# Kernel tuning notes

Measured on AMD Instinct MI355X. Metric: run time of the kernel, lower is better.

Reference implementation:

```python
import jax, jax.numpy as jnp
from jax import lax
import numpy as np

B, IN, HID, OUT, E = 32768, 512, 1024, 2, 64
N_MEM, N_ITER = 100, 10


def setup_inputs() -> dict:
    key = jax.random.key(0)
    ks = jax.random.split(key, 10)
    x = jax.random.normal(ks[0], (B, IN), dtype=jnp.float32)
    # encoder params (Linear stored as [in, out] for x @ W + b)
    e_w1 = jax.random.normal(ks[1], (IN, HID), dtype=jnp.float32) * 0.02
    e_b1 = jnp.zeros((HID,), dtype=jnp.float32)
    e_w2 = jax.random.normal(ks[2], (HID, E), dtype=jnp.float32) * 0.02
    e_b2 = jnp.zeros((E,), dtype=jnp.float32)
    # Hopfield weights: sum of outer products of N_MEM bipolar memories, zero diag, /N_MEM
    mems = jnp.where(jax.random.bernoulli(ks[3], 0.5, (N_MEM, E)), 1.0, -1.0)
    hop_w = (mems.T @ mems) / N_MEM
    hop_w = hop_w * (1.0 - jnp.eye(E, dtype=jnp.float32))
    # Q-network params
    n_w1 = jax.random.normal(ks[4], (IN + E, HID), dtype=jnp.float32) * 0.02
    n_b1 = jnp.zeros((HID,), dtype=jnp.float32)
    n_w2 = jax.random.normal(ks[5], (HID, HID), dtype=jnp.float32) * 0.02
    n_b2 = jnp.zeros((HID,), dtype=jnp.float32)
    n_w3 = jax.random.normal(ks[6], (HID, OUT), dtype=jnp.float32) * 0.02
    n_b3 = jnp.zeros((OUT,), dtype=jnp.float32)
    return {"x": x, "e_w1": e_w1, "e_b1": e_b1, "e_w2": e_w2, "e_b2": e_b2,
            "hop_w": hop_w, "n_w1": n_w1, "n_b1": n_b1, "n_w2": n_w2,
            "n_b2": n_b2, "n_w3": n_w3, "n_b3": n_b3}


def _retrieve(probe, hop_w):
    # Asynchronous Hopfield retrieval, batched over B.
    # probe: [B, E]; state in {+1,-1}
    state = jnp.where(probe > 0, 1.0, -1.0)
    idxs = jnp.arange(E)

    def unit_step(state, xs):
        i, w_row = xs  # w_row: [E]
        act = state @ w_row  # [B]
        state = state.at[:, i].set(jnp.where(act > 0, 1.0, -1.0))
        return state, None

    def iter_body(state, _):
        state, _ = lax.scan(unit_step, state, (idxs, hop_w))
        return state, None

    state, _ = lax.scan(iter_body, state, None, length=N_ITER)
    return jnp.where(state > 0, 1.0, 0.0)


def reference(x, e_w1, e_b1, e_w2, e_b2, hop_w, n_w1, n_b1, n_w2, n_b2, n_w3, n_b3):
    encoded = jax.nn.relu(x @ e_w1 + e_b1) @ e_w2 + e_b2  # [B, E]
    retrieved = lax.stop_gradient(_retrieve(encoded, hop_w))  # detached in original
    combined = jnp.concatenate([x, retrieved], axis=1)  # [B, IN+E]
    h = jax.nn.relu(combined @ n_w1 + n_b1)
    h = jax.nn.relu(h @ n_w2 + n_b2)
    return h @ n_w3 + n_b3  # [B, OUT]
```

## Files before the change

kernel.cpp:

```cpp
#include <hip/hip_runtime.h>
#include <hip/hip_bf16.h>
#include <stdint.h>
#include <math.h>

typedef __attribute__((ext_vector_type(4))) float f32x4;
typedef __attribute__((ext_vector_type(8))) __bf16 bf16x8;
typedef __attribute__((ext_vector_type(8))) uint16_t u16x8;
typedef __attribute__((ext_vector_type(4))) uint32_t u32x4;

__device__ __forceinline__ uint16_t f2bf(float f) {
  union { float f; uint32_t u; } v; v.f = f;
  uint32_t r = v.u + 0x7FFFu + ((v.u >> 16) & 1u);
  return (uint16_t)(r >> 16);
}
__device__ __forceinline__ float bf2f(uint16_t b) {
  union { uint32_t u; float f; } v; v.u = ((uint32_t)b) << 16;
  return v.f;
}

__global__ __launch_bounds__(256) void k_conv_x(const float* __restrict__ x,
                                                uint16_t* __restrict__ comb) {
  int i = blockIdx.x * 256 + threadIdx.x;
  int base = i * 8;
  int row = base >> 9;
  int col = base & 511;
  const float* src = x + base;
  f32x4 a = *(const f32x4*)src;
  f32x4 b = *(const f32x4*)(src + 4);
  u16x8 o;
  o[0] = f2bf(a[0]); o[1] = f2bf(a[1]); o[2] = f2bf(a[2]); o[3] = f2bf(a[3]);
  o[4] = f2bf(b[0]); o[5] = f2bf(b[1]); o[6] = f2bf(b[2]); o[7] = f2bf(b[3]);
  *(u16x8*)(comb + (size_t)row * 576 + col) = o;
}

__global__ __launch_bounds__(256) void k_convT(const float* __restrict__ W,
                                               uint16_t* __restrict__ WT,
                                               int K, int N) {
  int i = blockIdx.x * 256 + threadIdx.x;
  if (i < K * N) {
    int k = i / N, n = i % N;
    WT[n * K + k] = f2bf(W[i]);
  }
}

__global__ __launch_bounds__(256) void k_conv(const float* __restrict__ W,
                                              uint16_t* __restrict__ O, int n) {
  int i = blockIdx.x * 256 + threadIdx.x;
  if (i < n) O[i] = f2bf(W[i]);
}

template <int K, bool RELU>
__global__ __launch_bounds__(256)
void k_enc(const float* __restrict__ A, const float* __restrict__ W,
           const float* __restrict__ bias, float* __restrict__ C, int N) {
  __shared__ __align__(16) float xs[64][136];
  __shared__ __align__(16) float ws[64][68];
  const int t = threadIdx.x;
  const int m0 = blockIdx.y * 128, n0 = blockIdx.x * 64;
  const int mg = t >> 4, ng = t & 15;

  float res[8][4], acc[8][4];
#pragma unroll
  for (int i = 0; i < 8; ++i)
#pragma unroll
    for (int j = 0; j < 4; ++j) { res[i][j] = 0.f; acc[i][j] = 0.f; }

  const int xr = t >> 1, xk = (t & 1) * 32;
  const int wrr = t >> 2, wj = (t & 3) * 16;

  for (int c = 0; c < K / 64; ++c) {
    const int k0 = c * 64;
    if (k0 > 0 && (k0 % 384) == 0) {
#pragma unroll
      for (int i = 0; i < 8; ++i)
#pragma unroll
        for (int j = 0; j < 4; ++j) { res[i][j] += acc[i][j]; acc[i][j] = 0.f; }
    }
    __syncthreads();
#pragma unroll
    for (int u = 0; u < 8; ++u) {
      f32x4 v = *(const f32x4*)(A + (size_t)(m0 + xr) * K + k0 + xk + u * 4);
      xs[xk + u * 4 + 0][xr] = v[0];
      xs[xk + u * 4 + 1][xr] = v[1];
      xs[xk + u * 4 + 2][xr] = v[2];
      xs[xk + u * 4 + 3][xr] = v[3];
    }
#pragma unroll
    for (int u = 0; u < 4; ++u)
      *(f32x4*)&ws[wrr][wj + u * 4] =
          *(const f32x4*)(W + (size_t)(k0 + wrr) * N + n0 + wj + u * 4);
    __syncthreads();
#pragma unroll
    for (int k = 0; k < 64; ++k) {
      f32x4 x0 = *(const f32x4*)&xs[k][mg * 8];
      f32x4 x1 = *(const f32x4*)&xs[k][mg * 8 + 4];
      f32x4 wv = *(const f32x4*)&ws[k][ng * 4];
#pragma unroll
      for (int j = 0; j < 4; ++j) {
        acc[0][j] = fmaf(x0[0], wv[j], acc[0][j]);
        acc[1][j] = fmaf(x0[1], wv[j], acc[1][j]);
        acc[2][j] = fmaf(x0[2], wv[j], acc[2][j]);
        acc[3][j] = fmaf(x0[3], wv[j], acc[3][j]);
        acc[4][j] = fmaf(x1[0], wv[j], acc[4][j]);
        acc[5][j] = fmaf(x1[1], wv[j], acc[5][j]);
        acc[6][j] = fmaf(x1[2], wv[j], acc[6][j]);
        acc[7][j] = fmaf(x1[3], wv[j], acc[7][j]);
      }
    }
  }
#pragma unroll
  for (int i = 0; i < 8; ++i)
#pragma unroll
    for (int j = 0; j < 4; ++j) res[i][j] += acc[i][j];

#pragma unroll
  for (int i = 0; i < 8; ++i) {
    f32x4 o;
#pragma unroll
    for (int j = 0; j < 4; ++j) {
      float v = res[i][j] + bias[n0 + ng * 4 + j];
      if (RELU) v = fmaxf(v, 0.f);
      o[j] = v;
    }
    *(f32x4*)(C + (size_t)(m0 + mg * 8 + i) * N + n0 + ng * 4) = o;
  }
}

#define KNIFE_TAU 1e-6f

__device__ __forceinline__ void retrieve8(float (&s)[8],
                                          const float (*w)[64], int l) {
  for (int it = 0; it < 10; ++it) {
    bool changed = false;
#pragma unroll
    for (int i = 0; i < 64; ++i) {
      float r = 0.f;
#pragma unroll
      for (int c = 0; c < 8; ++c)
        r = fmaf(s[c], w[i][8 * c + l], r);
      r += __shfl_xor(r, 1);
      r += __shfl_xor(r, 2);
      r += __shfl_xor(r, 4);
      float ns = r > 0.f ? 1.f : -1.f;
      bool own = ((i & 7) == l);
      float cur = s[i >> 3];
      float nv = own ? ns : cur;
      changed |= (nv != cur);
      s[i >> 3] = nv;
    }
    if (!__any(changed)) break;
  }
}

__device__ __forceinline__ uint64_t gather_mask(const float (&s)[8], int g) {
  uint64_t m = 0;
#pragma unroll
  for (int c = 0; c < 8; ++c) {
    unsigned long long b = __ballot(s[c] > 0.f);
    m |= (uint64_t)((b >> (g * 8)) & 0xFFull) << (8 * c);
  }
  return m;
}

__global__ __launch_bounds__(256) void k_hopfield(const float* __restrict__ enc,
                                                  const float* __restrict__ hw,
                                                  uint16_t* __restrict__ comb) {
  __shared__ __align__(16) float w[64][64];
  const int t = threadIdx.x;
#pragma unroll
  for (int i = 0; i < 4; ++i)
    ((f32x4*)&w[0][0])[t * 4 + i] = ((const f32x4*)hw)[t * 4 + i];
  __syncthreads();

  const int lane = t & 63, wv = t >> 6;
  const int g = lane >> 3, l = lane & 7;
  const int sid = (blockIdx.x * 4 + wv) * 8 + g;
  const float* er = enc + (size_t)sid * 64;

  uint32_t imask = 0;
  int kc = -1;
  bool kpos = false;
#pragma unroll
  for (int c = 0; c < 8; ++c) {
    float v = er[8 * c + l];
    if (v > 0.f) imask |= (1u << c);
    if (kc < 0 && fabsf(v) < KNIFE_TAU) { kc = c; kpos = v > 0.f; }
  }
  unsigned long long kb = __ballot(kc >= 0);
  uint32_t gbits = (uint32_t)((kb >> (g * 8)) & 0xFFull);
  bool hasknife = gbits != 0;
  int klane = g * 8 + (__ffs(gbits) - 1);
  bool is_kl = hasknife && (lane == klane);
  uint32_t kbit = (kc >= 0) ? (1u << (kc & 7)) : 0u;

  uint32_t ma_bits = is_kl ? (imask | kbit) : imask;
  float sA[8];
#pragma unroll
  for (int c = 0; c < 8; ++c) sA[c] = ((ma_bits >> c) & 1u) ? 1.f : -1.f;
  retrieve8(sA, w, l);
  uint64_t mA = gather_mask(sA, g);
  uint64_t m = mA;

  if (__any(hasknife)) {
    if (hasknife) {
      uint32_t mb_bits = is_kl ? (imask & ~kbit) : imask;
      float sB[8];
#pragma unroll
      for (int c = 0; c < 8; ++c) sB[c] = ((mb_bits >> c) & 1u) ? 1.f : -1.f;
      retrieve8(sB, w, l);
      uint64_t mB = gather_mask(sB, g);
      if (mA != mB) {
        int kp = __shfl(kpos ? 1 : 0, klane);
        m = kp ? mA : mB;
      }
    }
  }

  uint32_t byte = (uint32_t)((m >> (8 * l)) & 0xFFull);
  u32x4 o;
#pragma unroll
  for (int p = 0; p < 4; ++p) {
    uint32_t lo = ((byte >> (2 * p)) & 1u) ? 0x3F80u : 0u;
    uint32_t hi = ((byte >> (2 * p + 1)) & 1u) ? 0x3F800000u : 0u;
    o[p] = lo | hi;
  }
  *(u32x4*)(comb + (size_t)sid * 576 + 512 + l * 8) = o;
}

__global__ __launch_bounds__(256)
void k_gemm_bf16(const uint16_t* __restrict__ A, const uint16_t* __restrict__ BT,
                 const float* __restrict__ bias, uint16_t* __restrict__ C,
                 int M, int N, int K, int relu) {
  constexpr int BM = 128, BN = 128, BK = 32;
  __shared__ __align__(16) uint16_t As[BM][BK];
  __shared__ __align__(16) uint16_t Bs[BN][BK];
  const int t = threadIdx.x;
  const int lane = t & 63, wid = t >> 6;
  const int wr = wid >> 1, wc = wid & 1;
  const int bm = blockIdx.y * BM, bn = blockIdx.x * BN;

  f32x4 acc[4][4] = {};

  const int s_row = t >> 1, s_kh = (t & 1) * 16;
  const uint16_t* Ag = A + (size_t)(bm + s_row) * K + s_kh;
  const uint16_t* Bg = BT + (size_t)(bn + s_row) * K + s_kh;
  const int l15 = lane & 15, kb = (lane >> 4) * 8;

  for (int kt = 0; kt < K / BK; ++kt) {
    __syncthreads();
    u16x8 av0 = *(const u16x8*)(Ag + kt * BK);
    u16x8 av1 = *(const u16x8*)(Ag + kt * BK + 8);
    u16x8 bv0 = *(const u16x8*)(Bg + kt * BK);
    u16x8 bv1 = *(const u16x8*)(Bg + kt * BK + 8);
    *(u16x8*)&As[s_row][s_kh] = av0;
    *(u16x8*)&As[s_row][s_kh + 8] = av1;
    *(u16x8*)&Bs[s_row][s_kh] = bv0;
    *(u16x8*)&Bs[s_row][s_kh + 8] = bv1;
    __syncthreads();
    bf16x8 af[4], bf[4];
#pragma unroll
    for (int m = 0; m < 4; ++m)
      af[m] = *(const bf16x8*)&As[wr * 64 + m * 16 + l15][kb];
#pragma unroll
    for (int n = 0; n < 4; ++n)
      bf[n] = *(const bf16x8*)&Bs[wc * 64 + n * 16 + l15][kb];
#pragma unroll
    for (int m = 0; m < 4; ++m)
#pragma unroll
      for (int n = 0; n < 4; ++n)
        acc[m][n] = __builtin_amdgcn_mfma_f32_16x16x32_bf16(af[m], bf[n],
                                                            acc[m][n], 0, 0, 0);
  }
#pragma unroll
  for (int m = 0; m < 4; ++m) {
    int row = bm + wr * 64 + m * 16 + (lane >> 4) * 4;
#pragma unroll
    for (int n = 0; n < 4; ++n) {
      int col = bn + wc * 64 + n * 16 + l15;
      float bsv = bias[col];
#pragma unroll
      for (int r = 0; r < 4; ++r) {
        float v = acc[m][n][r] + bsv;
        if (relu) v = fmaxf(v, 0.f);
        C[(size_t)(row + r) * N + col] = f2bf(v);
      }
    }
  }
}

__global__ __launch_bounds__(256) void k_n3(const uint16_t* __restrict__ h2,
                                            const uint16_t* __restrict__ w3,
                                            const float* __restrict__ b3,
                                            float* __restrict__ out, int M) {
  const int lane = threadIdx.x & 63;
  const int wglob = (blockIdx.x * 256 + threadIdx.x) >> 6;
  const int nw = (gridDim.x * 256) >> 6;
  u16x8 wa = *(const u16x8*)(w3 + lane * 16);
  u16x8 wb = *(const u16x8*)(w3 + lane * 16 + 8);
  u16x8 wc = *(const u16x8*)(w3 + 1024 + lane * 16);
  u16x8 wd = *(const u16x8*)(w3 + 1024 + lane * 16 + 8);
  const float b0 = b3[0], b1 = b3[1];
  for (int row = wglob; row < M; row += nw) {
    const uint16_t* hr = h2 + (size_t)row * 1024;
    u16x8 h0 = *(const u16x8*)(hr + lane * 8);
    u16x8 h1 = *(const u16x8*)(hr + 512 + lane * 8);
    float a0 = 0.f, a1 = 0.f;
#pragma unroll
    for (int e = 0; e < 4; ++e) {
      float h = bf2f(h0[e]);
      a0 = fmaf(h, bf2f(wa[2 * e]), a0);
      a1 = fmaf(h, bf2f(wa[2 * e + 1]), a1);
    }
#pragma unroll
    for (int e = 4; e < 8; ++e) {
      float h = bf2f(h0[e]);
      a0 = fmaf(h, bf2f(wb[2 * e - 8]), a0);
      a1 = fmaf(h, bf2f(wb[2 * e - 7]), a1);
    }
#pragma unroll
    for (int e = 0; e < 4; ++e) {
      float h = bf2f(h1[e]);
      a0 = fmaf(h, bf2f(wc[2 * e]), a0);
      a1 = fmaf(h, bf2f(wc[2 * e + 1]), a1);
    }
#pragma unroll
    for (int e = 4; e < 8; ++e) {
      float h = bf2f(h1[e]);
      a0 = fmaf(h, bf2f(wd[2 * e - 8]), a0);
      a1 = fmaf(h, bf2f(wd[2 * e - 7]), a1);
    }
#pragma unroll
    for (int off = 32; off; off >>= 1) {
      a0 += __shfl_xor(a0, off, 64);
      a1 += __shfl_xor(a1, off, 64);
    }
    if (lane == 0) {
      out[(size_t)row * 2 + 0] = a0 + b0;
      out[(size_t)row * 2 + 1] = a1 + b1;
    }
  }
}

extern "C" void kernel_launch(void* const* d_in, const int* in_sizes, int n_in,
                              void* d_out, int out_size, void* d_ws, size_t ws_size,
                              hipStream_t stream) {
  const float* x     = (const float*)d_in[0];
  const float* e_w1  = (const float*)d_in[1];
  const float* e_b1  = (const float*)d_in[2];
  const float* e_w2  = (const float*)d_in[3];
  const float* e_b2  = (const float*)d_in[4];
  const float* hop_w = (const float*)d_in[5];
  const float* n_w1  = (const float*)d_in[6];
  const float* n_b1  = (const float*)d_in[7];
  const float* n_w2  = (const float*)d_in[8];
  const float* n_b2  = (const float*)d_in[9];
  const float* n_w3  = (const float*)d_in[10];
  const float* n_b3  = (const float*)d_in[11];
  float* out = (float*)d_out;
  char* ws = (char*)d_ws;

  float*    h1e  = (float*)(ws + 0);
  uint16_t* h1   = (uint16_t*)(ws + 0);
  uint16_t* h2   = (uint16_t*)(ws + 67108864);
  uint16_t* comb = (uint16_t*)(ws + 134217728);
  float*    enc  = (float*)(ws + 171966464);
  uint16_t* w1t  = (uint16_t*)(ws + 180355072);
  uint16_t* w2t  = (uint16_t*)(ws + 181534720);
  uint16_t* w3b  = (uint16_t*)(ws + 183631872);

  k_conv_x<<<8192, 256, 0, stream>>>(x, comb);
  k_convT<<<(576 * 1024 + 255) / 256, 256, 0, stream>>>(n_w1, w1t, 576, 1024);
  k_convT<<<(1024 * 1024 + 255) / 256, 256, 0, stream>>>(n_w2, w2t, 1024, 1024);
  k_conv<<<(2048 + 255) / 256, 256, 0, stream>>>(n_w3, w3b, 2048);

  k_enc<512, true><<<dim3(1024 / 64, 32768 / 128), 256, 0, stream>>>(
      x, e_w1, e_b1, h1e, 1024);
  k_enc<1024, false><<<dim3(1, 32768 / 128), 256, 0, stream>>>(
      h1e, e_w2, e_b2, enc, 64);

  k_hopfield<<<32768 / 32, 256, 0, stream>>>(enc, hop_w, comb);

  k_gemm_bf16<<<dim3(1024 / 128, 32768 / 128), 256, 0, stream>>>(
      comb, w1t, n_b1, h1, 32768, 1024, 576, 1);
  k_gemm_bf16<<<dim3(1024 / 128, 32768 / 128), 256, 0, stream>>>(
      h1, w2t, n_b2, h2, 32768, 1024, 1024, 1);
  k_n3<<<512, 256, 0, stream>>>(h2, w3b, n_b3, out, 32768);
}
```

Measured before the change: 1.194 ms.

## Tile weight transposes, register-prefetch encoder tiles, and use direct-to-LDS loads in GEMM

The weight transpose-convert kernel now goes through a padded shared-memory tile, so both its global reads and its writes are coalesced instead of scattered. The fp32 encoder GEMM prefetches the next K-chunk into registers while the current chunk is being computed, hiding global-load latency. The bf16 MFMA GEMM replaces its global-to-register-to-LDS staging with global_load_lds 16-byte direct-to-LDS loads, which saves VGPRs and instructions. The direct LDS writes use a contiguous unpadded layout, which may cause LDS bank conflicts, and the register prefetch raises register pressure in the encoder kernel.

```diff
diff --git a/kernel.cpp b/kernel.cpp
--- a/kernel.cpp
+++ b/kernel.cpp
@@ -16,6 +16,11 @@
 __device__ __forceinline__ float bf2f(uint16_t b) {
   union { uint32_t u; float f; } v; v.u = ((uint32_t)b) << 16;
   return v.f;
+}
+__device__ __forceinline__ void gload16(const void* g, void* l) {
+  __builtin_amdgcn_global_load_lds(
+      (const __attribute__((address_space(1))) uint32_t*)g,
+      (__attribute__((address_space(3))) uint32_t*)l, 16, 0, 0);
 }
 
 __global__ __launch_bounds__(256) void k_conv_x(const float* __restrict__ x,
@@ -36,10 +41,20 @@
 __global__ __launch_bounds__(256) void k_convT(const float* __restrict__ W,
                                                uint16_t* __restrict__ WT,
                                                int K, int N) {
-  int i = blockIdx.x * 256 + threadIdx.x;
-  if (i < K * N) {
-    int k = i / N, n = i % N;
-    WT[n * K + k] = f2bf(W[i]);
+  __shared__ float tile[64][65];
+  const int t = threadIdx.x;
+  const int n0 = blockIdx.x * 64, k0 = blockIdx.y * 64;
+  const int c = t & 63, r0 = t >> 6;
+#pragma unroll
+  for (int rr = 0; rr < 16; ++rr) {
+    int r = r0 * 16 + rr;
+    tile[r][c] = W[(size_t)(k0 + r) * N + n0 + c];
+  }
+  __syncthreads();
+#pragma unroll
+  for (int rr = 0; rr < 16; ++rr) {
+    int r = r0 * 16 + rr;
+    WT[(size_t)(n0 + r) * K + k0 + c] = f2bf(tile[c][r]);
   }
 }
 
@@ -68,28 +83,43 @@
   const int xr = t >> 1, xk = (t & 1) * 32;
   const int wrr = t >> 2, wj = (t & 3) * 16;
 
-  for (int c = 0; c < K / 64; ++c) {
+  f32x4 pa[8], pb[4];
+  const float* Arow = A + (size_t)(m0 + xr) * K + xk;
+  const float* Wrow = W + (size_t)wrr * N + n0 + wj;
+
+#pragma unroll
+  for (int u = 0; u < 8; ++u) pa[u] = *(const f32x4*)(Arow + u * 4);
+#pragma unroll
+  for (int u = 0; u < 4; ++u) pb[u] = *(const f32x4*)(Wrow + u * 4);
+
+  constexpr int NT = K / 64;
+  for (int c = 0; c < NT; ++c) {
     const int k0 = c * 64;
+    __syncthreads();
+#pragma unroll
+    for (int u = 0; u < 8; ++u) {
+      xs[xk + u * 4 + 0][xr] = pa[u][0];
+      xs[xk + u * 4 + 1][xr] = pa[u][1];
+      xs[xk + u * 4 + 2][xr] = pa[u][2];
+      xs[xk + u * 4 + 3][xr] = pa[u][3];
+    }
+#pragma unroll
+    for (int u = 0; u < 4; ++u) *(f32x4*)&ws[wrr][wj + u * 4] = pb[u];
+    __syncthreads();
+    if (c + 1 < NT) {
+      const float* An = Arow + (c + 1) * 64;
+      const float* Wn = W + (size_t)((c + 1) * 64 + wrr) * N + n0 + wj;
+#pragma unroll
+      for (int u = 0; u < 8; ++u) pa[u] = *(const f32x4*)(An + u * 4);
+#pragma unroll
+      for (int u = 0; u < 4; ++u) pb[u] = *(const f32x4*)(Wn + u * 4);
+    }
     if (k0 > 0 && (k0 % 384) == 0) {
 #pragma unroll
       for (int i = 0; i < 8; ++i)
 #pragma unroll
         for (int j = 0; j < 4; ++j) { res[i][j] += acc[i][j]; acc[i][j] = 0.f; }
     }
-    __syncthreads();
-#pragma unroll
-    for (int u = 0; u < 8; ++u) {
-      f32x4 v = *(const f32x4*)(A + (size_t)(m0 + xr) * K + k0 + xk + u * 4);
-      xs[xk + u * 4 + 0][xr] = v[0];
-      xs[xk + u * 4 + 1][xr] = v[1];
-      xs[xk + u * 4 + 2][xr] = v[2];
-      xs[xk + u * 4 + 3][xr] = v[3];
-    }
-#pragma unroll
-    for (int u = 0; u < 4; ++u)
-      *(f32x4*)&ws[wrr][wj + u * 4] =
-          *(const f32x4*)(W + (size_t)(k0 + wrr) * N + n0 + wj + u * 4);
-    __syncthreads();
 #pragma unroll
     for (int k = 0; k < 64; ++k) {
       f32x4 x0 = *(const f32x4*)&xs[k][mg * 8];
@@ -241,21 +271,24 @@
 
   f32x4 acc[4][4] = {};
 
-  const int s_row = t >> 1, s_kh = (t & 1) * 16;
-  const uint16_t* Ag = A + (size_t)(bm + s_row) * K + s_kh;
-  const uint16_t* Bg = BT + (size_t)(bn + s_row) * K + s_kh;
   const int l15 = lane & 15, kb = (lane >> 4) * 8;
+  const int i0 = t, i1 = t + 256;
+  const int r0 = i0 >> 2, c0 = (i0 & 3) * 8;
+  const int r1 = i1 >> 2, c1 = (i1 & 3) * 8;
+  const uint16_t* A0 = A + (size_t)(bm + r0) * K + c0;
+  const uint16_t* A1 = A + (size_t)(bm + r1) * K + c1;
+  const uint16_t* B0 = BT + (size_t)(bn + r0) * K + c0;
+  const uint16_t* B1 = BT + (size_t)(bn + r1) * K + c1;
+  uint16_t* Al = &As[0][0];
+  uint16_t* Bl = &Bs[0][0];
 
   for (int kt = 0; kt < K / BK; ++kt) {
     __syncthreads();
-    u16x8 av0 = *(const u16x8*)(Ag + kt * BK);
-    u16x8 av1 = *(const u16x8*)(Ag + kt * BK + 8);
-    u16x8 bv0 = *(const u16x8*)(Bg + kt * BK);
-    u16x8 bv1 = *(const u16x8*)(Bg + kt * BK + 8);
-    *(u16x8*)&As[s_row][s_kh] = av0;
-    *(u16x8*)&As[s_row][s_kh + 8] = av1;
-    *(u16x8*)&Bs[s_row][s_kh] = bv0;
-    *(u16x8*)&Bs[s_row][s_kh + 8] = bv1;
+    const int ko = kt * BK;
+    gload16(A0 + ko, Al + i0 * 8);
+    gload16(A1 + ko, Al + i1 * 8);
+    gload16(B0 + ko, Bl + i0 * 8);
+    gload16(B1 + ko, Bl + i1 * 8);
     __syncthreads();
     bf16x8 af[4], bf[4];
 #pragma unroll
@@ -369,8 +402,8 @@
   uint16_t* w3b  = (uint16_t*)(ws + 183631872);
 
   k_conv_x<<<8192, 256, 0, stream>>>(x, comb);
-  k_convT<<<(576 * 1024 + 255) / 256, 256, 0, stream>>>(n_w1, w1t, 576, 1024);
-  k_convT<<<(1024 * 1024 + 255) / 256, 256, 0, stream>>>(n_w2, w2t, 1024, 1024);
+  k_convT<<<dim3(1024 / 64, 576 / 64), 256, 0, stream>>>(n_w1, w1t, 576, 1024);
+  k_convT<<<dim3(1024 / 64, 1024 / 64), 256, 0, stream>>>(n_w2, w2t, 1024, 1024);
   k_conv<<<(2048 + 255) / 256, 256, 0, stream>>>(n_w3, w3b, 2048);
 
   k_enc<512, true><<<dim3(1024 / 64, 32768 / 128), 256, 0, stream>>>(
```

New measurement: 1.263 ms. 5.7% more time.
